# Performance work log

Measured on AMD Instinct MI355X. Metric: run time of the kernel, lower is better.

## Reference

```python
import jax, jax.numpy as jnp
import numpy as np

B, C, CI, H, W = 4, 64, 32, 96, 96  # batch, in_channels, inter_channels, spatial
EPS = 1e-5


def conv1x1(x, w, b):
    # x: [B,Cin,H,W], w: [Cout,Cin], b: [Cout]
    return jnp.einsum('bchw,oc->bohw', x, w) + b[None, :, None, None]


def maxpool2(x):
    b, c, h, w = x.shape
    return x.reshape(b, c, h // 2, 2, w // 2, 2).max(axis=(3, 5))


def setup_inputs() -> dict:
    key = jax.random.key(0)
    ks = jax.random.split(key, 12)
    s = 0.05  # keep unscaled attention logits in a sane range
    return {
        'x': jax.random.normal(ks[0], (B, C, H, W), jnp.float32),
        'feature': jax.random.normal(ks[1], (B, CI, H, W), jnp.float32),
        'g_w': jax.random.normal(ks[2], (C, C), jnp.float32) * s,
        'g_b': jax.random.normal(ks[3], (C,), jnp.float32) * s,
        'theta_w': jax.random.normal(ks[4], (C, C), jnp.float32) * s,
        'theta_b': jax.random.normal(ks[5], (C,), jnp.float32) * s,
        'phi_w': jax.random.normal(ks[6], (C, CI), jnp.float32) * s,
        'phi_b': jax.random.normal(ks[7], (C,), jnp.float32) * s,
        'W_w': jax.random.normal(ks[8], (CI, C), jnp.float32) * s,
        'W_b': jax.random.normal(ks[9], (CI,), jnp.float32) * s,
        'bn_gamma': jax.random.normal(ks[10], (CI,), jnp.float32) * s + 1.0,
        'bn_beta': jax.random.normal(ks[11], (CI,), jnp.float32) * s,
    }


def reference(x, feature, g_w, g_b, theta_w, theta_b, phi_w, phi_b, W_w, W_b, bn_gamma, bn_beta):
    b = x.shape[0]
    # g branch: conv1x1 then 2x2 maxpool -> [B, M, C]
    g_x = maxpool2(conv1x1(x, g_w, g_b)).reshape(b, C, -1).transpose(0, 2, 1)
    # theta: conv1x1 -> [B, N, C]
    theta_x = conv1x1(x, theta_w, theta_b).reshape(b, C, -1).transpose(0, 2, 1)
    # phi on `feature` (inter_channels -> in_channels) then maxpool -> [B, C, M]
    phi_f = maxpool2(conv1x1(feature, phi_w, phi_b)).reshape(b, C, -1)
    # unscaled attention: [B, N, M]
    f = jnp.einsum('bnc,bcm->bnm', theta_x, phi_f)
    f_div_C = jax.nn.softmax(f, axis=-1)
    y = jnp.einsum('bnm,bmc->bnc', f_div_C, g_x)  # [B, N, C]
    y = y.transpose(0, 2, 1).reshape(x.shape)
    z = y + x
    # W: conv1x1 (C -> CI) + BatchNorm2d (training mode, batch stats)
    z = conv1x1(z, W_w, W_b)
    mean = z.mean(axis=(0, 2, 3), keepdims=True)
    var = z.var(axis=(0, 2, 3), keepdims=True)
    z = (z - mean) * jax.lax.rsqrt(var + EPS)
    z = z * bn_gamma[None, :, None, None] + bn_beta[None, :, None, None]
    return z
```

## Files before the change

kernel.cpp:

```cpp
#include <hip/hip_runtime.h>
#include <hip/hip_bf16.h>

typedef __attribute__((ext_vector_type(8))) short short8;
typedef __attribute__((ext_vector_type(4))) float f32x4;
typedef __attribute__((ext_vector_type(4))) _Float16 half4;

#define NB 4
#define NN 9216
#define NM 2304

__device__ inline unsigned pk2(float a, float b) {
  __hip_bfloat16 ha = __float2bfloat16(a), hb = __float2bfloat16(b);
  return (unsigned)*(unsigned short*)&ha | ((unsigned)*(unsigned short*)&hb << 16);
}
__device__ inline float ubf(unsigned u) {
  unsigned v = u << 16; return *(float*)&v;
}
__device__ inline short8 pack8(const float* v) {
  short8 s;
#pragma unroll
  for (int j = 0; j < 8; ++j) { __hip_bfloat16 h = __float2bfloat16(v[j]); s[j] = *(short*)&h; }
  return s;
}
__device__ inline short8 ldw8(const float* p) {
  float tmp[8];
  *(float4*)&tmp[0] = *(const float4*)p;
  *(float4*)&tmp[4] = *(const float4*)(p + 4);
  return pack8(tmp);
}

__global__ __launch_bounds__(256) void conv_pool_k(
    const float* __restrict__ x, const float* __restrict__ feat,
    const float* __restrict__ tw, const float* __restrict__ tbi,
    const float* __restrict__ gw, const float* __restrict__ gbi,
    const float* __restrict__ pw, const float* __restrict__ pbi,
    __hip_bfloat16* __restrict__ Theta, _Float16* __restrict__ Gcm,
    __hip_bfloat16* __restrict__ PhiT, float* __restrict__ psum) {
  int t = threadIdx.x, wv = t >> 6, lane = t & 63, l15 = lane & 15, q = lane >> 4;
  int b = blockIdx.y, bx = blockIdx.x;
  if (bx == 0 && b == 0 && t < 64) psum[t] = 0.f;
  int jt = bx % 6, rp = bx / 6;
  int i0 = rp * 2, j0 = jt * 16;
  int ntop = i0 * 96 + j0;
  int ot = wv;

  short8 wt[2], wg[2], wp1;
#pragma unroll
  for (int kf = 0; kf < 2; ++kf) {
    wt[kf] = ldw8(tw + (size_t)(ot * 16 + l15) * 64 + kf * 32 + q * 8);
    wg[kf] = ldw8(gw + (size_t)(ot * 16 + l15) * 64 + kf * 32 + q * 8);
  }
  wp1 = ldw8(pw + (size_t)(ot * 16 + l15) * 32 + q * 8);

  short8 bxf[2][2], bff[2];
  {
    float tmp[8];
#pragma unroll
    for (int row = 0; row < 2; ++row) {
#pragma unroll
      for (int kf = 0; kf < 2; ++kf) {
#pragma unroll
        for (int j = 0; j < 8; ++j)
          tmp[j] = x[((size_t)b * 64 + kf * 32 + q * 8 + j) * NN + ntop + row * 96 + l15];
        bxf[row][kf] = pack8(tmp);
      }
#pragma unroll
      for (int j = 0; j < 8; ++j)
        tmp[j] = feat[((size_t)b * 32 + q * 8 + j) * NN + ntop + row * 96 + l15];
      bff[row] = pack8(tmp);
    }
  }

  int m = rp * 48 + ((j0 + l15) >> 1);
  bool em = (l15 & 1) == 0;

#pragma unroll
  for (int row = 0; row < 2; ++row) {
    f32x4 d;
#pragma unroll
    for (int r = 0; r < 4; ++r) d[r] = tbi[ot * 16 + q * 4 + r];
    d = __builtin_amdgcn_mfma_f32_16x16x32_bf16(wt[0], bxf[row][0], d, 0, 0, 0);
    d = __builtin_amdgcn_mfma_f32_16x16x32_bf16(wt[1], bxf[row][1], d, 0, 0, 0);
    size_t base = ((size_t)b * NN + ntop + row * 96 + l15) * 64 + ot * 16 + q * 4;
    *(unsigned*)(Theta + base) = pk2(d[0], d[1]);
    *(unsigned*)(Theta + base + 2) = pk2(d[2], d[3]);
  }
  {
    f32x4 d0, d1;
#pragma unroll
    for (int r = 0; r < 4; ++r) { float bb = gbi[ot * 16 + q * 4 + r]; d0[r] = bb; d1[r] = bb; }
    d0 = __builtin_amdgcn_mfma_f32_16x16x32_bf16(wg[0], bxf[0][0], d0, 0, 0, 0);
    d0 = __builtin_amdgcn_mfma_f32_16x16x32_bf16(wg[1], bxf[0][1], d0, 0, 0, 0);
    d1 = __builtin_amdgcn_mfma_f32_16x16x32_bf16(wg[0], bxf[1][0], d1, 0, 0, 0);
    d1 = __builtin_amdgcn_mfma_f32_16x16x32_bf16(wg[1], bxf[1][1], d1, 0, 0, 0);
    float h[4];
#pragma unroll
    for (int r = 0; r < 4; ++r) {
      float v = fmaxf(d0[r], d1[r]);
      h[r] = fmaxf(v, __shfl_xor(v, 1));
    }
    if (em) {
#pragma unroll
      for (int r = 0; r < 4; ++r)
        Gcm[((size_t)b * 64 + ot * 16 + q * 4 + r) * NM + m] = (_Float16)h[r];
    }
  }
  {
    f32x4 d0, d1;
#pragma unroll
    for (int r = 0; r < 4; ++r) { float bb = pbi[ot * 16 + q * 4 + r]; d0[r] = bb; d1[r] = bb; }
    d0 = __builtin_amdgcn_mfma_f32_16x16x32_bf16(wp1, bff[0], d0, 0, 0, 0);
    d1 = __builtin_amdgcn_mfma_f32_16x16x32_bf16(wp1, bff[1], d1, 0, 0, 0);
    float h[4];
#pragma unroll
    for (int r = 0; r < 4; ++r) {
      float v = fmaxf(d0[r], d1[r]);
      h[r] = fmaxf(v, __shfl_xor(v, 1));
    }
    if (em) {
      size_t base = ((size_t)b * NM + m) * 64 + ot * 16 + q * 4;
      *(unsigned*)(PhiT + base) = pk2(h[0], h[1]);
      *(unsigned*)(PhiT + base + 2) = pk2(h[2], h[3]);
    }
  }
}

__global__ __launch_bounds__(256, 4) void attn_k(
    const __hip_bfloat16* __restrict__ Theta, const __hip_bfloat16* __restrict__ PhiT,
    const _Float16* __restrict__ Gcm, const float* __restrict__ x,
    const float* __restrict__ Ww, const float* __restrict__ Wb,
    float* __restrict__ z2, float* __restrict__ psum) {
  __shared__ union {
    struct { __hip_bfloat16 phis[2][64][72]; _Float16 gs[2][64][72]; } st;
    struct { __hip_bfloat16 zpart[4][48][68]; __hip_bfloat16 zacc[48][72]; } ep;
  } u;
  __shared__ float rs[4][64];

  int t = threadIdx.x, wv = t >> 6, lane = t & 63;
  int l15 = lane & 15, q = lane >> 4;
  int b = blockIdx.y;
  int n0 = blockIdx.x * 48;

  short8 tb[3][2];
#pragma unroll
  for (int nt = 0; nt < 3; ++nt)
#pragma unroll
    for (int kf = 0; kf < 2; ++kf)
      tb[nt][kf] = *(const short8*)(Theta + ((size_t)b * NN + n0 + nt * 16 + l15) * 64 + kf * 32 + q * 8);

  f32x4 acc[3][4];
#pragma unroll
  for (int nt = 0; nt < 3; ++nt)
#pragma unroll
    for (int ct = 0; ct < 4; ++ct) acc[nt][ct] = (f32x4){0.f, 0.f, 0.f, 0.f};
  float rsum[3] = {0.f, 0.f, 0.f};

  const __hip_bfloat16* phibase = PhiT + (size_t)b * NM * 64;
  const _Float16* gbase = Gcm + (size_t)b * 64 * NM;

  int pr = t >> 3, pseg = t & 7;
  uint4 rphi[2], rg[2];

#pragma unroll
  for (int p = 0; p < 2; ++p)
    rphi[p] = *(const uint4*)(phibase + (size_t)(p * 32 + pr) * 64 + pseg * 8);
#pragma unroll
  for (int p = 0; p < 2; ++p)
    rg[p] = *(const uint4*)(gbase + (size_t)(p * 32 + pr) * NM + pseg * 8);
#pragma unroll
  for (int p = 0; p < 2; ++p)
    *(uint4*)&u.st.phis[0][p * 32 + pr][pseg * 8] = rphi[p];
#pragma unroll
  for (int p = 0; p < 2; ++p)
    *(uint4*)&u.st.gs[0][p * 32 + pr][pseg * 8] = rg[p];

  for (int ck = 0; ck < NM / 64; ++ck) {
    int cur = ck & 1;
    __syncthreads();

    if (ck < 35) {
      int m1 = (ck + 1) * 64;
#pragma unroll
      for (int p = 0; p < 2; ++p)
        rphi[p] = *(const uint4*)(phibase + (size_t)(m1 + p * 32 + pr) * 64 + pseg * 8);
#pragma unroll
      for (int p = 0; p < 2; ++p)
        rg[p] = *(const uint4*)(gbase + (size_t)(p * 32 + pr) * NM + m1 + pseg * 8);
    }

    short8 pha[2];
#pragma unroll
    for (int kf = 0; kf < 2; ++kf)
      pha[kf] = *(const short8*)&u.st.phis[cur][wv * 16 + l15][kf * 32 + q * 8];
    half4 gv[4];
#pragma unroll
    for (int ct = 0; ct < 4; ++ct)
      gv[ct] = *(const half4*)&u.st.gs[cur][ct * 16 + l15][wv * 16 + q * 4];

    half4 pa[3];
#pragma unroll
    for (int nt = 0; nt < 3; ++nt) {
      f32x4 s = (f32x4){0.f, 0.f, 0.f, 0.f};
      s = __builtin_amdgcn_mfma_f32_16x16x32_bf16(pha[0], tb[nt][0], s, 0, 0, 0);
      s = __builtin_amdgcn_mfma_f32_16x16x32_bf16(pha[1], tb[nt][1], s, 0, 0, 0);
      float e0 = __expf(s[0]), e1 = __expf(s[1]), e2 = __expf(s[2]), e3 = __expf(s[3]);
      rsum[nt] += (e0 + e1) + (e2 + e3);
      pa[nt] = (half4){(_Float16)e0, (_Float16)e1, (_Float16)e2, (_Float16)e3};
    }
#pragma unroll
    for (int nt = 0; nt < 3; ++nt)
#pragma unroll
      for (int ct = 0; ct < 4; ++ct)
        acc[nt][ct] = __builtin_amdgcn_mfma_f32_16x16x16f16(pa[nt], gv[ct], acc[nt][ct], 0, 0, 0);

    if (ck < 35) {
#pragma unroll
      for (int p = 0; p < 2; ++p)
        *(uint4*)&u.st.phis[cur ^ 1][p * 32 + pr][pseg * 8] = rphi[p];
#pragma unroll
      for (int p = 0; p < 2; ++p)
        *(uint4*)&u.st.gs[cur ^ 1][p * 32 + pr][pseg * 8] = rg[p];
    }
  }

#pragma unroll
  for (int nt = 0; nt < 3; ++nt) {
    float v = rsum[nt];
    v += __shfl_xor(v, 16);
    v += __shfl_xor(v, 32);
    if (lane < 16) rs[wv][nt * 16 + lane] = v;
  }
  __syncthreads();

#pragma unroll
  for (int nt = 0; nt < 3; ++nt)
#pragma unroll
    for (int ct = 0; ct < 4; ++ct)
#pragma unroll
      for (int r = 0; r < 4; ++r)
        u.ep.zpart[wv][nt * 16 + q * 4 + r][ct * 16 + l15] = __float2bfloat16(acc[nt][ct][r]);
  __syncthreads();

  if (wv < 3) {
    int row = wv * 16 + l15;
    float tot = rs[0][row] + rs[1][row] + rs[2][row] + rs[3][row];
    float rinv = 1.0f / tot;
    float ys[16];
#pragma unroll
    for (int j4 = 0; j4 < 4; ++j4) {
      uint2 p0 = *(const uint2*)&u.ep.zpart[0][row][q * 16 + j4 * 4];
      ys[j4 * 4 + 0] = ubf(p0.x & 0xffffu); ys[j4 * 4 + 1] = ubf(p0.x >> 16);
      ys[j4 * 4 + 2] = ubf(p0.y & 0xffffu); ys[j4 * 4 + 3] = ubf(p0.y >> 16);
    }
#pragma unroll
    for (int wvv = 1; wvv < 4; ++wvv) {
#pragma unroll
      for (int j4 = 0; j4 < 4; ++j4) {
        uint2 p0 = *(const uint2*)&u.ep.zpart[wvv][row][q * 16 + j4 * 4];
        ys[j4 * 4 + 0] += ubf(p0.x & 0xffffu); ys[j4 * 4 + 1] += ubf(p0.x >> 16);
        ys[j4 * 4 + 2] += ubf(p0.y & 0xffffu); ys[j4 * 4 + 3] += ubf(p0.y >> 16);
      }
    }
    float z1[16];
#pragma unroll
    for (int i = 0; i < 16; ++i)
      z1[i] = ys[i] * rinv + x[((size_t)b * 64 + q * 16 + i) * NN + n0 + row];
#pragma unroll
    for (int i2 = 0; i2 < 8; ++i2)
      *(unsigned*)&u.ep.zacc[row][q * 16 + 2 * i2] = pk2(z1[2 * i2], z1[2 * i2 + 1]);
  }
  __syncthreads();

  f32x4 dd[2];
  if (wv < 3) {
    int nw = n0 + wv * 16;
    short8 wbf[2][2];
#pragma unroll
    for (int ot = 0; ot < 2; ++ot)
#pragma unroll
      for (int kf = 0; kf < 2; ++kf)
        wbf[ot][kf] = ldw8(Ww + (size_t)(ot * 16 + l15) * 64 + kf * 32 + q * 8);
    short8 za0 = *(const short8*)&u.ep.zacc[wv * 16 + l15][q * 8];
    short8 za1 = *(const short8*)&u.ep.zacc[wv * 16 + l15][32 + q * 8];

#pragma unroll
    for (int ot = 0; ot < 2; ++ot) {
      float bias = Wb[ot * 16 + l15];
      f32x4 d = (f32x4){bias, bias, bias, bias};
      d = __builtin_amdgcn_mfma_f32_16x16x32_bf16(za0, wbf[ot][0], d, 0, 0, 0);
      d = __builtin_amdgcn_mfma_f32_16x16x32_bf16(za1, wbf[ot][1], d, 0, 0, 0);
#pragma unroll
      for (int r = 0; r < 4; ++r)
        z2[((size_t)b * NN + nw + q * 4 + r) * 32 + ot * 16 + l15] = d[r];
      dd[ot] = d;
    }
  }

  __syncthreads();
  if (wv < 3) {
#pragma unroll
    for (int ot = 0; ot < 2; ++ot) {
      float ps = (dd[ot][0] + dd[ot][1]) + (dd[ot][2] + dd[ot][3]);
      float ps2 = dd[ot][0] * dd[ot][0] + dd[ot][1] * dd[ot][1] +
                  dd[ot][2] * dd[ot][2] + dd[ot][3] * dd[ot][3];
      ps += __shfl_xor(ps, 16);  ps += __shfl_xor(ps, 32);
      ps2 += __shfl_xor(ps2, 16); ps2 += __shfl_xor(ps2, 32);
      if (lane < 16) {
        rs[wv][ot * 16 + lane] = ps;
        rs[wv][32 + ot * 16 + lane] = ps2;
      }
    }
  }
  __syncthreads();
  if (t < 64) {
    float tot = rs[0][t] + rs[1][t] + rs[2][t];
    atomicAdd(&psum[t], tot);
  }
}

__global__ __launch_bounds__(256) void bn_apply(
    const float* __restrict__ z2, const float* __restrict__ psum,
    const float* __restrict__ gamma, const float* __restrict__ beta,
    float* __restrict__ out) {
  __shared__ float ssl[64];
  __shared__ float zt[32][65];
  int t = threadIdx.x, b = blockIdx.y, n0 = blockIdx.x * 64;
  if (t < 32) {
    const float inv = 1.0f / (float)(NB * NN);
    float mean = psum[t] * inv;
    float var = psum[32 + t] * inv - mean * mean;
    float sc = gamma[t] * rsqrtf(var + 1e-5f);
    ssl[t] = sc;
    ssl[32 + t] = beta[t] - mean * sc;
  }
#pragma unroll
  for (int it = 0; it < 2; ++it) {
    int idx = it * 256 + t, r = idx >> 3, seg = idx & 7;
    float4 vv = *(const float4*)(z2 + ((size_t)b * NN + n0 + r) * 32 + seg * 4);
    zt[seg * 4 + 0][r] = vv.x; zt[seg * 4 + 1][r] = vv.y;
    zt[seg * 4 + 2][r] = vv.z; zt[seg * 4 + 3][r] = vv.w;
  }
  __syncthreads();
  int o = t >> 3, nseg = t & 7;
  float sc = ssl[o], sh = ssl[32 + o];
  float4 a, c;
  a.x = zt[o][nseg * 8 + 0] * sc + sh; a.y = zt[o][nseg * 8 + 1] * sc + sh;
  a.z = zt[o][nseg * 8 + 2] * sc + sh; a.w = zt[o][nseg * 8 + 3] * sc + sh;
  c.x = zt[o][nseg * 8 + 4] * sc + sh; c.y = zt[o][nseg * 8 + 5] * sc + sh;
  c.z = zt[o][nseg * 8 + 6] * sc + sh; c.w = zt[o][nseg * 8 + 7] * sc + sh;
  float* po = out + ((size_t)b * 32 + o) * NN + n0 + nseg * 8;
  *(float4*)po = a;
  *(float4*)(po + 4) = c;
}

extern "C" void kernel_launch(void* const* d_in, const int* in_sizes, int n_in,
                              void* d_out, int out_size, void* d_ws, size_t ws_size,
                              hipStream_t stream) {
  const float* x       = (const float*)d_in[0];
  const float* feature = (const float*)d_in[1];
  const float* g_w     = (const float*)d_in[2];
  const float* g_b     = (const float*)d_in[3];
  const float* theta_w = (const float*)d_in[4];
  const float* theta_b = (const float*)d_in[5];
  const float* phi_w   = (const float*)d_in[6];
  const float* phi_b   = (const float*)d_in[7];
  const float* W_w     = (const float*)d_in[8];
  const float* W_b     = (const float*)d_in[9];
  const float* bn_g    = (const float*)d_in[10];
  const float* bn_b    = (const float*)d_in[11];

  char* ws = (char*)d_ws;
  __hip_bfloat16* Theta = (__hip_bfloat16*)(ws);
  _Float16*       Gcm   = (_Float16*)(ws + 4718592);
  __hip_bfloat16* PhiT  = (__hip_bfloat16*)(ws + 5898240);
  float*          z2    = (float*)(ws + 7077888);
  float*          psum  = (float*)(ws + 11796480);

  conv_pool_k<<<dim3(288, NB), dim3(256), 0, stream>>>(
      x, feature, theta_w, theta_b, g_w, g_b, phi_w, phi_b, Theta, Gcm, PhiT, psum);
  attn_k<<<dim3(192, NB), dim3(256), 0, stream>>>(
      Theta, PhiT, Gcm, x, W_w, W_b, z2, psum);
  bn_apply<<<dim3(144, NB), dim3(256), 0, stream>>>(
      z2, psum, bn_g, bn_b, (float*)d_out);
}
```

Baseline: 148.7 us.

## Load attention phi/g operands directly from global into registers, drop LDS staging

Each wave now reads its own phi and g MFMA fragments from global memory into double-buffered registers, replacing the cooperative LDS staging and the per-chunk __syncthreads. The shared union becomes just the epilogue buffers, and launch bounds drop from 4 to 3 waves-per-SIMD to leave room for the extra registers. The aim is to remove LDS write/read traffic and block-wide barriers in the main loop. In exchange, each wave issues narrower, less coalesced global loads (the g loads are strided by NM), and occupancy may fall.

New measurement: 180.9 us. 1.22x slower.

```diff
diff --git a/kernel.cpp b/kernel.cpp
--- a/kernel.cpp
+++ b/kernel.cpp
@@ -125,15 +125,15 @@
   }
 }
 
-__global__ __launch_bounds__(256, 4) void attn_k(
+__global__ __launch_bounds__(256, 3) void attn_k(
     const __hip_bfloat16* __restrict__ Theta, const __hip_bfloat16* __restrict__ PhiT,
     const _Float16* __restrict__ Gcm, const float* __restrict__ x,
     const float* __restrict__ Ww, const float* __restrict__ Wb,
     float* __restrict__ z2, float* __restrict__ psum) {
-  __shared__ union {
-    struct { __hip_bfloat16 phis[2][64][72]; _Float16 gs[2][64][72]; } st;
-    struct { __hip_bfloat16 zpart[4][48][68]; __hip_bfloat16 zacc[48][72]; } ep;
-  } u;
+  __shared__ struct {
+    __hip_bfloat16 zpart[4][48][68];
+    __hip_bfloat16 zacc[48][72];
+  } ep;
   __shared__ float rs[4][64];
 
   int t = threadIdx.x, wv = t >> 6, lane = t & 63;
@@ -155,54 +155,38 @@
     for (int ct = 0; ct < 4; ++ct) acc[nt][ct] = (f32x4){0.f, 0.f, 0.f, 0.f};
   float rsum[3] = {0.f, 0.f, 0.f};
 
-  const __hip_bfloat16* phibase = PhiT + (size_t)b * NM * 64;
-  const _Float16* gbase = Gcm + (size_t)b * 64 * NM;
-
-  int pr = t >> 3, pseg = t & 7;
-  uint4 rphi[2], rg[2];
-
-#pragma unroll
-  for (int p = 0; p < 2; ++p)
-    rphi[p] = *(const uint4*)(phibase + (size_t)(p * 32 + pr) * 64 + pseg * 8);
-#pragma unroll
-  for (int p = 0; p < 2; ++p)
-    rg[p] = *(const uint4*)(gbase + (size_t)(p * 32 + pr) * NM + pseg * 8);
-#pragma unroll
-  for (int p = 0; p < 2; ++p)
-    *(uint4*)&u.st.phis[0][p * 32 + pr][pseg * 8] = rphi[p];
-#pragma unroll
-  for (int p = 0; p < 2; ++p)
-    *(uint4*)&u.st.gs[0][p * 32 + pr][pseg * 8] = rg[p];
-
+  const __hip_bfloat16* phiw = PhiT + (size_t)b * NM * 64 + (size_t)(wv * 16 + l15) * 64 + q * 8;
+  const _Float16* gw0 = Gcm + (size_t)b * 64 * NM + wv * 16 + q * 4;
+
+  short8 pha[2][2];
+  half4 gv[2][4];
+
+#pragma unroll
+  for (int kf = 0; kf < 2; ++kf)
+    pha[0][kf] = *(const short8*)(phiw + kf * 32);
+#pragma unroll
+  for (int ct = 0; ct < 4; ++ct)
+    gv[0][ct] = *(const half4*)(gw0 + (size_t)(ct * 16 + l15) * NM);
+
+#pragma unroll 2
   for (int ck = 0; ck < NM / 64; ++ck) {
     int cur = ck & 1;
-    __syncthreads();
-
     if (ck < 35) {
       int m1 = (ck + 1) * 64;
 #pragma unroll
-      for (int p = 0; p < 2; ++p)
-        rphi[p] = *(const uint4*)(phibase + (size_t)(m1 + p * 32 + pr) * 64 + pseg * 8);
-#pragma unroll
-      for (int p = 0; p < 2; ++p)
-        rg[p] = *(const uint4*)(gbase + (size_t)(p * 32 + pr) * NM + m1 + pseg * 8);
-    }
-
-    short8 pha[2];
-#pragma unroll
-    for (int kf = 0; kf < 2; ++kf)
-      pha[kf] = *(const short8*)&u.st.phis[cur][wv * 16 + l15][kf * 32 + q * 8];
-    half4 gv[4];
-#pragma unroll
-    for (int ct = 0; ct < 4; ++ct)
-      gv[ct] = *(const half4*)&u.st.gs[cur][ct * 16 + l15][wv * 16 + q * 4];
+      for (int kf = 0; kf < 2; ++kf)
+        pha[cur ^ 1][kf] = *(const short8*)(phiw + (size_t)m1 * 64 + kf * 32);
+#pragma unroll
+      for (int ct = 0; ct < 4; ++ct)
+        gv[cur ^ 1][ct] = *(const half4*)(gw0 + (size_t)(ct * 16 + l15) * NM + m1);
+    }
 
     half4 pa[3];
 #pragma unroll
     for (int nt = 0; nt < 3; ++nt) {
       f32x4 s = (f32x4){0.f, 0.f, 0.f, 0.f};
-      s = __builtin_amdgcn_mfma_f32_16x16x32_bf16(pha[0], tb[nt][0], s, 0, 0, 0);
-      s = __builtin_amdgcn_mfma_f32_16x16x32_bf16(pha[1], tb[nt][1], s, 0, 0, 0);
+      s = __builtin_amdgcn_mfma_f32_16x16x32_bf16(pha[cur][0], tb[nt][0], s, 0, 0, 0);
+      s = __builtin_amdgcn_mfma_f32_16x16x32_bf16(pha[cur][1], tb[nt][1], s, 0, 0, 0);
       float e0 = __expf(s[0]), e1 = __expf(s[1]), e2 = __expf(s[2]), e3 = __expf(s[3]);
       rsum[nt] += (e0 + e1) + (e2 + e3);
       pa[nt] = (half4){(_Float16)e0, (_Float16)e1, (_Float16)e2, (_Float16)e3};
@@ -211,16 +195,7 @@
     for (int nt = 0; nt < 3; ++nt)
 #pragma unroll
       for (int ct = 0; ct < 4; ++ct)
-        acc[nt][ct] = __builtin_amdgcn_mfma_f32_16x16x16f16(pa[nt], gv[ct], acc[nt][ct], 0, 0, 0);
-
-    if (ck < 35) {
-#pragma unroll
-      for (int p = 0; p < 2; ++p)
-        *(uint4*)&u.st.phis[cur ^ 1][p * 32 + pr][pseg * 8] = rphi[p];
-#pragma unroll
-      for (int p = 0; p < 2; ++p)
-        *(uint4*)&u.st.gs[cur ^ 1][p * 32 + pr][pseg * 8] = rg[p];
-    }
+        acc[nt][ct] = __builtin_amdgcn_mfma_f32_16x16x16f16(pa[nt], gv[cur][ct], acc[nt][ct], 0, 0, 0);
   }
 
 #pragma unroll
@@ -230,7 +205,6 @@
     v += __shfl_xor(v, 32);
     if (lane < 16) rs[wv][nt * 16 + lane] = v;
   }
-  __syncthreads();
 
 #pragma unroll
   for (int nt = 0; nt < 3; ++nt)
@@ -238,7 +212,7 @@
     for (int ct = 0; ct < 4; ++ct)
 #pragma unroll
       for (int r = 0; r < 4; ++r)
-        u.ep.zpart[wv][nt * 16 + q * 4 + r][ct * 16 + l15] = __float2bfloat16(acc[nt][ct][r]);
+        ep.zpart[wv][nt * 16 + q * 4 + r][ct * 16 + l15] = __float2bfloat16(acc[nt][ct][r]);
   __syncthreads();
 
   if (wv < 3) {
@@ -248,7 +222,7 @@
     float ys[16];
 #pragma unroll
     for (int j4 = 0; j4 < 4; ++j4) {
-      uint2 p0 = *(const uint2*)&u.ep.zpart[0][row][q * 16 + j4 * 4];
+      uint2 p0 = *(const uint2*)&ep.zpart[0][row][q * 16 + j4 * 4];
       ys[j4 * 4 + 0] = ubf(p0.x & 0xffffu); ys[j4 * 4 + 1] = ubf(p0.x >> 16);
       ys[j4 * 4 + 2] = ubf(p0.y & 0xffffu); ys[j4 * 4 + 3] = ubf(p0.y >> 16);
     }
@@ -256,7 +230,7 @@
     for (int wvv = 1; wvv < 4; ++wvv) {
 #pragma unroll
       for (int j4 = 0; j4 < 4; ++j4) {
-        uint2 p0 = *(const uint2*)&u.ep.zpart[wvv][row][q * 16 + j4 * 4];
+        uint2 p0 = *(const uint2*)&ep.zpart[wvv][row][q * 16 + j4 * 4];
         ys[j4 * 4 + 0] += ubf(p0.x & 0xffffu); ys[j4 * 4 + 1] += ubf(p0.x >> 16);
         ys[j4 * 4 + 2] += ubf(p0.y & 0xffffu); ys[j4 * 4 + 3] += ubf(p0.y >> 16);
       }
@@ -267,7 +241,7 @@
       z1[i] = ys[i] * rinv + x[((size_t)b * 64 + q * 16 + i) * NN + n0 + row];
 #pragma unroll
     for (int i2 = 0; i2 < 8; ++i2)
-      *(unsigned*)&u.ep.zacc[row][q * 16 + 2 * i2] = pk2(z1[2 * i2], z1[2 * i2 + 1]);
+      *(unsigned*)&ep.zacc[row][q * 16 + 2 * i2] = pk2(z1[2 * i2], z1[2 * i2 + 1]);
   }
   __syncthreads();
 
@@ -280,8 +254,8 @@
 #pragma unroll
       for (int kf = 0; kf < 2; ++kf)
         wbf[ot][kf] = ldw8(Ww + (size_t)(ot * 16 + l15) * 64 + kf * 32 + q * 8);
-    short8 za0 = *(const short8*)&u.ep.zacc[wv * 16 + l15][q * 8];
-    short8 za1 = *(const short8*)&u.ep.zacc[wv * 16 + l15][32 + q * 8];
+    short8 za0 = *(const short8*)&ep.zacc[wv * 16 + l15][q * 8];
+    short8 za1 = *(const short8*)&ep.zacc[wv * 16 + l15][32 + q * 8];
 
 #pragma unroll
     for (int ot = 0; ot < 2; ++ot) {
```
